# Optimization experiments

Hardware: AMD Instinct MI355X
Metric: run time of the kernel (lower is better)

The kernel has to match this reference:

```python
import jax, jax.numpy as jnp
import numpy as np

NOPE, ROPE, VDIM, QKD = 128, 64, 128, 192
H = 16
EPS = 1e-6
SCALING = QKD ** -0.5


def rms_norm(x, w):
    xf = x.astype(jnp.float32)
    var = jnp.mean(xf * xf, axis=-1, keepdims=True)
    return (w * (xf * jax.lax.rsqrt(var + EPS))).astype(x.dtype)


def rotate_half(x):
    d = x.shape[-1] // 2
    return jnp.concatenate((-x[..., d:], x[..., :d]), axis=-1)


def apply_rope(q, k, cos, sin):
    # cos/sin: [B,S,D] -> unsqueeze head dim
    cos = cos[:, None, :, :]
    sin = sin[:, None, :, :]
    return q * cos + rotate_half(q) * sin, k * cos + rotate_half(k) * sin


def setup_inputs() -> dict:
    key = jax.random.key(0)
    ks = jax.random.split(key, 8)
    B, S, D = 2, 2048, 2048
    pos = jnp.arange(S, dtype=jnp.float32)
    inv_freq = 1.0 / (10000.0 ** (jnp.arange(0, ROPE, 2, dtype=jnp.float32) / ROPE))
    ang = pos[:, None] * inv_freq[None, :]            # [S, ROPE/2]
    emb = jnp.concatenate([ang, ang], axis=-1)        # [S, ROPE]
    cos = jnp.broadcast_to(jnp.cos(emb)[None], (B, S, ROPE))
    sin = jnp.broadcast_to(jnp.sin(emb)[None], (B, S, ROPE))
    s = lambda k, shp, fan: jax.random.normal(k, shp, jnp.float32) * (fan ** -0.5)
    return {
        "hidden_states": jax.random.normal(ks[0], (B, S, D), jnp.float32),
        "cos": cos,
        "sin": sin,
        "q_a_W": s(ks[1], (1536, D), D),
        "q_a_norm_w": jnp.ones((1536,), jnp.float32),
        "q_b_W": s(ks[2], (H * QKD, 1536), 1536),
        "kv_a_W": s(ks[3], (512 + ROPE, D), D),
        "kv_a_norm_w": jnp.ones((512,), jnp.float32),
        "kv_b_W": s(ks[4], (H * (NOPE + VDIM), 512), 512),
        "o_W": s(ks[5], (D, H * VDIM), H * VDIM),
    }


def reference(hidden_states, cos, sin, q_a_W, q_a_norm_w, q_b_W, kv_a_W,
              kv_a_norm_w, kv_b_W, o_W):
    B, S, D = hidden_states.shape
    # low-rank Q path
    q = rms_norm(hidden_states @ q_a_W.T, q_a_norm_w) @ q_b_W.T   # [B,S,H*QKD]
    q = q.reshape(B, S, H, QKD).transpose(0, 2, 1, 3)             # [B,H,S,QKD]
    q_pass, q_rot = q[..., :NOPE], q[..., NOPE:]
    # compressed KV path
    ckv = hidden_states @ kv_a_W.T                                # [B,S,512+ROPE]
    k_lat, k_rot = ckv[..., :512], ckv[..., 512:]
    kv = rms_norm(k_lat, kv_a_norm_w) @ kv_b_W.T                  # [B,S,H*(NOPE+VDIM)]
    kv = kv.reshape(B, S, H, NOPE + VDIM).transpose(0, 2, 1, 3)   # [B,H,S,*]
    k_pass, v = kv[..., :NOPE], kv[..., NOPE:]
    k_rot = k_rot.reshape(B, 1, S, ROPE)
    q_rot, k_rot = apply_rope(q_rot, k_rot, cos, sin)
    k_rot = jnp.broadcast_to(k_rot, (B, H, S, ROPE))
    query = jnp.concatenate((q_pass, q_rot), axis=-1)             # [B,H,S,QKD]
    key = jnp.concatenate((k_pass, k_rot), axis=-1)
    # eager causal attention
    scores = jnp.einsum('bhsd,bhtd->bhst', query, key) * SCALING
    causal = jnp.tril(jnp.ones((S, S), bool))
    scores = jnp.where(causal, scores, jnp.finfo(scores.dtype).min)
    attn = jax.nn.softmax(scores.astype(jnp.float32), axis=-1).astype(query.dtype)
    out = jnp.einsum('bhst,bhtd->bhsd', attn, v)                  # [B,H,S,VDIM]
    out = out.transpose(0, 2, 1, 3).reshape(B, S, H * VDIM)
    return out @ o_W.T
```

## Files before the change

### kernel.cpp

```cpp
#include <hip/hip_runtime.h>
#include <hip/hip_bf16.h>


typedef __bf16 bf16x8 __attribute__((ext_vector_type(8)));
typedef float floatx4 __attribute__((ext_vector_type(4)));
#define BF16 __hip_bfloat16

static __device__ __forceinline__ BF16 f2b(float x) { return __float2bfloat16(x); }
static __device__ __forceinline__ unsigned short b2u(BF16 x) { return *(unsigned short*)&x; }
static __device__ __forceinline__ float fast_exp2(float x) { return __builtin_amdgcn_exp2f(x); }

template<int CTRL>
static __device__ __forceinline__ float dpp_mov(float x) {
  int xi = __builtin_bit_cast(int, x);
  int yi = __builtin_amdgcn_update_dpp(xi, xi, CTRL, 0xF, 0xF, false);
  return __builtin_bit_cast(float, yi);
}
static __device__ __forceinline__ float row_allmax(float x) {
  x = fmaxf(x, dpp_mov<0xB1>(x));
  x = fmaxf(x, dpp_mov<0x4E>(x));
  x = fmaxf(x, dpp_mov<0x141>(x));
  x = fmaxf(x, dpp_mov<0x140>(x));
  return x;
}
static __device__ __forceinline__ float row_allsum(float x) {
  x += dpp_mov<0xB1>(x);
  x += dpp_mov<0x4E>(x);
  x += dpp_mov<0x141>(x);
  x += dpp_mov<0x140>(x);
  return x;
}

static __device__ __forceinline__ void load_lds16(const BF16* g, BF16* l) {
  __builtin_amdgcn_global_load_lds((__attribute__((address_space(1))) void*)(void*)g,
                                   (__attribute__((address_space(3))) void*)(void*)l,
                                   16, 0, 0);
}

struct CastArgs {
  const float* src[6];
  BF16* dst[6];
  long n[6];
};
__global__ void cast_multi_k(CastArgs a) {
  int r = blockIdx.y;
  long n = a.n[r];
  const float* __restrict__ x = a.src[r];
  BF16* __restrict__ y = a.dst[r];
  for (long i = ((long)blockIdx.x * 256 + threadIdx.x) * 4; i + 3 < n;
       i += (long)gridDim.x * 1024) {
    float4 v = *(const float4*)(x + i);
    y[i+0] = f2b(v.x); y[i+1] = f2b(v.y); y[i+2] = f2b(v.z); y[i+3] = f2b(v.w);
  }
}

template<int OUT_MODE>
static __device__ __forceinline__ void gemm_body(
    const BF16* __restrict__ A, const BF16* __restrict__ B, void* __restrict__ C,
    int M, int N, int K, const float* __restrict__ cosb, const float* __restrict__ sinb,
    BF16* __restrict__ P1, BF16* __restrict__ P2, int bx, int by, BF16* As, BF16* Bs) {
  int tid = threadIdx.x, wave = tid >> 6, lane = tid & 63;
  int wr = wave >> 1, wc = wave & 1, lr = lane & 15, quad = lane >> 4;
  long m0 = (long)by * 128, n0 = (long)bx * 128;

  int c0 = wave*64 + lane, c1 = c0 + 256;
  const BF16* ga0 = A + (m0 + (c0>>2))*(long)K + (c0&3)*8;
  const BF16* ga1 = A + (m0 + (c1>>2))*(long)K + (c1&3)*8;
  long bn0 = n0 + (c0>>2); if (bn0 >= N) bn0 = N-1;
  long bn1 = n0 + (c1>>2); if (bn1 >= N) bn1 = N-1;
  const BF16* gb0 = B + bn0*(long)K + (c0&3)*8;
  const BF16* gb1 = B + bn1*(long)K + (c1&3)*8;
  BF16* la0 = As + wave*512;
  BF16* la1 = As + wave*512 + 2048;
  BF16* lb0 = Bs + wave*512;
  BF16* lb1 = Bs + wave*512 + 2048;

  floatx4 acc[4][4] = {};
  for (int k0 = 0; k0 < K; k0 += 32) {
    __syncthreads();
    load_lds16(ga0 + k0, la0);
    load_lds16(ga1 + k0, la1);
    load_lds16(gb0 + k0, lb0);
    load_lds16(gb1 + k0, lb1);
    __syncthreads();
    bf16x8 a[4], b[4];
#pragma unroll
    for (int i = 0; i < 4; i++) a[i] = *(const bf16x8*)(As + (wr*64 + i*16 + lr)*32 + quad*8);
#pragma unroll
    for (int j = 0; j < 4; j++) b[j] = *(const bf16x8*)(Bs + (wc*64 + j*16 + lr)*32 + quad*8);
#pragma unroll
    for (int i = 0; i < 4; i++)
#pragma unroll
      for (int j = 0; j < 4; j++)
        acc[i][j] = __builtin_amdgcn_mfma_f32_16x16x32_bf16(a[i], b[j], acc[i][j], 0, 0, 0);
  }

  long n0w = n0 + wc*64;
  const float SCALE_L2E = 0.104117546f;
#pragma unroll
  for (int i = 0; i < 4; i++) {
    long tok = m0 + wr*64 + i*16 + quad*4;
    long bb = tok >> 11, s = tok & 2047;
    if (OUT_MODE == 0) {
#pragma unroll
      for (int r = 0; r < 4; r++) {
        long row = tok + r;
#pragma unroll
        for (int j = 0; j < 4; j++) {
          long col = n0w + j*16 + lr;
          if (col < N) ((float*)C)[row*(long)N + col] = acc[i][j][r];
        }
      }
    } else if (OUT_MODE == 2) {
#pragma unroll
      for (int j = 0; j < 4; j++) {
        long col = n0w + j*16 + lr;
        long h = col >> 8, d = col & 255;
        if (d < 128) {
#pragma unroll
          for (int r = 0; r < 4; r++)
            P1[((bb*16 + h)*2048 + s + r)*192 + d] = f2b(acc[i][j][r]);
        } else {
          ushort4 pk;
          pk.x = b2u(f2b(acc[i][j][0])); pk.y = b2u(f2b(acc[i][j][1]));
          pk.z = b2u(f2b(acc[i][j][2])); pk.w = b2u(f2b(acc[i][j][3]));
          *(ushort4*)(P2 + ((bb*16 + h)*128 + d - 128)*2048 + s) = pk;
        }
      }
    } else {
      bool rope = ((n0w % 192) == 128);
#pragma unroll
      for (int r = 0; r < 4; r++) {
        long row = tok + r;
#pragma unroll
        for (int j = 0; j < 4; j++) {
          long col = n0w + j*16 + lr;
          float x = acc[i][j][r], val;
          if (rope) {
            int id = j*16 + lr;
            float partner = acc[i][j^2][r];
            float rot = (j < 2) ? -partner : partner;
            val = x*cosb[row*64 + id] + rot*sinb[row*64 + id];
          } else {
            val = x;
          }
          long h = col / 192, d = col % 192;
          P1[((bb*16 + h)*2048 + s + r)*192 + d] = f2b(val * SCALE_L2E);
        }
      }
    }
  }
}

__global__ __launch_bounds__(256) void gemm0_k(const BF16* __restrict__ A, const BF16* __restrict__ B,
                                               float* __restrict__ C, int M, int N, int K) {
  __shared__ __align__(16) BF16 As[128*32];
  __shared__ __align__(16) BF16 Bs[128*32];
  gemm_body<0>(A, B, C, M, N, K, nullptr, nullptr, nullptr, nullptr,
               blockIdx.x, blockIdx.y, As, Bs);
}

__global__ __launch_bounds__(256) void gemm_qkv_k(const BF16* __restrict__ qan, const BF16* __restrict__ Wqb,
                                                  const BF16* __restrict__ kvn, const BF16* __restrict__ Wkvb,
                                                  const float* __restrict__ cosb, const float* __restrict__ sinb,
                                                  BF16* __restrict__ Qt, BF16* __restrict__ Kt,
                                                  BF16* __restrict__ Vt) {
  __shared__ __align__(16) BF16 As[128*32];
  __shared__ __align__(16) BF16 Bs[128*32];
  int bid = blockIdx.x;
  if (bid < 768) {
    gemm_body<3>(qan, Wqb, nullptr, 4096, 3072, 1536, cosb, sinb, Qt, nullptr,
                 bid % 24, bid / 24, As, Bs);
  } else {
    bid -= 768;
    gemm_body<2>(kvn, Wkvb, nullptr, 4096, 4096, 512, nullptr, nullptr, Kt, Vt,
                 bid % 32, bid / 32, As, Bs);
  }
}

__global__ __launch_bounds__(256) void norms_k(const float* __restrict__ qakv,
                                               const float* __restrict__ qw, const float* __restrict__ kw,
                                               const float* __restrict__ cosb, const float* __restrict__ sinb,
                                               BF16* __restrict__ qan, BF16* __restrict__ kvn,
                                               BF16* __restrict__ Kt) {
  long row = blockIdx.x;
  const float* xr = qakv + row * 2112;
  int tid = threadIdx.x;
  __shared__ float red[4];
  {
    float ss = 0.f;
    for (int i = tid*4; i < 1536; i += 1024) {
      float4 v = *(const float4*)(xr + i);
      ss += v.x*v.x + v.y*v.y + v.z*v.z + v.w*v.w;
    }
#pragma unroll
    for (int off = 32; off > 0; off >>= 1) ss += __shfl_down(ss, off);
    if ((tid & 63) == 0) red[tid >> 6] = ss;
    __syncthreads();
    float rs = rsqrtf((red[0]+red[1]+red[2]+red[3]) / 1536.f + 1e-6f);
    BF16* yr = qan + row * 1536;
    for (int i = tid*4; i < 1536; i += 1024) {
      float4 v = *(const float4*)(xr + i);
      yr[i+0] = f2b(v.x * qw[i+0] * rs);
      yr[i+1] = f2b(v.y * qw[i+1] * rs);
      yr[i+2] = f2b(v.z * qw[i+2] * rs);
      yr[i+3] = f2b(v.w * qw[i+3] * rs);
    }
  }
  __syncthreads();
  {
    float ss = 0.f;
    for (int i = tid*4; i < 512; i += 1024) {
      float4 v = *(const float4*)(xr + 1536 + i);
      ss += v.x*v.x + v.y*v.y + v.z*v.z + v.w*v.w;
    }
#pragma unroll
    for (int off = 32; off > 0; off >>= 1) ss += __shfl_down(ss, off);
    if ((tid & 63) == 0) red[tid >> 6] = ss;
    __syncthreads();
    float rs = rsqrtf((red[0]+red[1]+red[2]+red[3]) / 512.f + 1e-6f);
    BF16* yr = kvn + row * 512;
    for (int i = tid*4; i < 512; i += 1024) {
      float4 v = *(const float4*)(xr + 1536 + i);
      yr[i+0] = f2b(v.x * kw[i+0] * rs);
      yr[i+1] = f2b(v.y * kw[i+1] * rs);
      yr[i+2] = f2b(v.z * kw[i+2] * rs);
      yr[i+3] = f2b(v.w * kw[i+3] * rs);
    }
  }
  if (tid < 64) {
    int i = tid;
    const float* kr = xr + 2048;
    float x = kr[i];
    float rot = (i < 32) ? -kr[i + 32] : kr[i - 32];
    BF16 v = f2b(x * cosb[row*64 + i] + rot * sinb[row*64 + i]);
    long b = row >> 11, s = row & 2047;
    long base = ((b*16)*2048 + s)*192 + 128 + i;
#pragma unroll
    for (int h = 0; h < 16; h++) Kt[base + (long)h*2048*192] = v;
  }
}

#define LK 200
#define LV 72
#define LP 72
__global__ __launch_bounds__(512) void flash_k(const BF16* __restrict__ Qt, const BF16* __restrict__ Kt,
                                               const BF16* __restrict__ Vt, BF16* __restrict__ O) {
  __shared__ __align__(16) BF16 Ks[64*LK];
  __shared__ __align__(16) BF16 Vs[128*LV];
  __shared__ __align__(16) BF16 Ps[8][16*LP];
  int tid = threadIdx.x, wave = tid >> 6, lane = tid & 63;
  int lr = lane & 15, quad = lane >> 4;
  int F = blockIdx.x;
  int g = F & 31, j = F >> 5;
  int h = g & 15, b = g >> 4;
  const BF16* Qb = Qt + ((long)(b*16 + h) * 2048) * 192;
  const BF16* Kb = Kt + ((long)(b*16 + h) * 2048) * 192;
  const BF16* Vb = Vt + ((long)(b*16 + h) * 128) * 2048;
  const float NEG_INF = -__builtin_inff();

  int krow[3], kcol[3];
#pragma unroll
  for (int i = 0; i < 3; i++) {
    int c = tid + 512*i;
    krow[i] = c / 24; kcol[i] = (c % 24) * 8;
  }
  int vrow[2], vcol[2];
#pragma unroll
  for (int i = 0; i < 2; i++) {
    int c = tid + 512*i;
    vrow[i] = c >> 3; vcol[i] = (c & 7) * 8;
  }

  bf16x8 kreg[3], vreg[2];
  auto stage_load = [&](int k0) {
#pragma unroll
    for (int i = 0; i < 3; i++)
      kreg[i] = *(const bf16x8*)(Kb + (long)(k0 + krow[i])*192 + kcol[i]);
#pragma unroll
    for (int i = 0; i < 2; i++)
      vreg[i] = *(const bf16x8*)(Vb + (long)vrow[i]*2048 + k0 + vcol[i]);
  };
  auto stage_store = [&]() {
#pragma unroll
    for (int i = 0; i < 3; i++)
      *(bf16x8*)(Ks + krow[i]*LK + kcol[i]) = kreg[i];
#pragma unroll
    for (int i = 0; i < 2; i++)
      *(bf16x8*)(Vs + vrow[i]*LV + vcol[i]) = vreg[i];
  };

  for (int half = 0; half < 2; half++) {
    int qt = (half == 0) ? j : 15 - j;
    int q0 = qt * 128;
    int wq0 = q0 + wave*16;
    bf16x8 qf[6];
    {
      const BF16* qp = Qb + (long)(wq0 + lr) * 192 + quad*8;
#pragma unroll
      for (int f = 0; f < 6; f++) qf[f] = *(const bf16x8*)(qp + f*32);
    }
    float m_i[4], l_i[4];
#pragma unroll
    for (int r = 0; r < 4; r++) { m_i[r] = NEG_INF; l_i[r] = 0.f; }
    floatx4 o_acc[8] = {};
    int nk = 2*qt + 2;
    stage_load(0);
    for (int kt = 0; kt < nk; kt++) {
      __syncthreads();
      stage_store();
      __syncthreads();
      if (kt + 1 < nk) stage_load((kt + 1) * 64);
      if (kt*64 > wq0 + 15) continue;
      floatx4 st[4];
#pragma unroll
      for (int t = 0; t < 4; t++) {
        floatx4 c = {};
#pragma unroll
        for (int f = 0; f < 6; f++) {
          bf16x8 kf = *(const bf16x8*)(Ks + (t*16+lr)*LK + f*32 + quad*8);
          c = __builtin_amdgcn_mfma_f32_16x16x32_bf16(qf[f], kf, c, 0, 0, 0);
        }
        st[t] = c;
      }
      float mt[4];
#pragma unroll
      for (int r = 0; r < 4; r++) mt[r] = NEG_INF;
      if (kt*64 + 63 > wq0) {
        int rbase = wq0 + quad*4 - kt*64;
#pragma unroll
        for (int t = 0; t < 4; t++) {
          int coff = t*16 + lr;
#pragma unroll
          for (int r = 0; r < 4; r++) {
            float sc = st[t][r];
            if (coff > rbase + r) sc = NEG_INF;
            st[t][r] = sc;
            mt[r] = fmaxf(mt[r], sc);
          }
        }
      } else {
#pragma unroll
        for (int t = 0; t < 4; t++)
#pragma unroll
          for (int r = 0; r < 4; r++) mt[r] = fmaxf(mt[r], st[t][r]);
      }
#pragma unroll
      for (int r = 0; r < 4; r++) mt[r] = row_allmax(mt[r]);
      float alpha[4], rsum[4];
#pragma unroll
      for (int r = 0; r < 4; r++) {
        float mn = fmaxf(m_i[r], mt[r]);
        alpha[r] = fast_exp2(m_i[r] - mn);
        m_i[r] = mn;
        rsum[r] = 0.f;
      }
#pragma unroll
      for (int t = 0; t < 4; t++)
#pragma unroll
        for (int r = 0; r < 4; r++) {
          float p = fast_exp2(st[t][r] - m_i[r]);
          st[t][r] = p;
          rsum[r] += p;
        }
#pragma unroll
      for (int r = 0; r < 4; r++) rsum[r] = row_allsum(rsum[r]);
#pragma unroll
      for (int r = 0; r < 4; r++) l_i[r] = l_i[r]*alpha[r] + rsum[r];
#pragma unroll
      for (int v = 0; v < 8; v++)
#pragma unroll
        for (int r = 0; r < 4; r++) o_acc[v][r] *= alpha[r];
#pragma unroll
      for (int t = 0; t < 4; t++)
#pragma unroll
        for (int r = 0; r < 4; r++)
          Ps[wave][(quad*4 + r)*LP + t*16 + lr] = f2b(st[t][r]);
#pragma unroll
      for (int kc = 0; kc < 2; kc++) {
        bf16x8 pa = *(const bf16x8*)(&Ps[wave][lr*LP + kc*32 + quad*8]);
#pragma unroll
        for (int v = 0; v < 8; v++) {
          bf16x8 vf = *(const bf16x8*)(&Vs[(v*16+lr)*LV + kc*32 + quad*8]);
          o_acc[v] = __builtin_amdgcn_mfma_f32_16x16x32_bf16(pa, vf, o_acc[v], 0, 0, 0);
        }
      }
    }
    long rowb = wq0 + quad*4;
#pragma unroll
    for (int v = 0; v < 8; v++)
#pragma unroll
      for (int r = 0; r < 4; r++) {
        long row = rowb + r;
        O[((long)b*2048 + row)*2048 + h*128 + v*16 + lr] = f2b(o_acc[v][r] / l_i[r]);
      }
  }
}

extern "C" void kernel_launch(void* const* d_in, const int* in_sizes, int n_in,
                              void* d_out, int out_size, void* d_ws, size_t ws_size,
                              hipStream_t stream) {
  const float* hidden      = (const float*)d_in[0];
  const float* cosb        = (const float*)d_in[1];
  const float* sinb        = (const float*)d_in[2];
  const float* q_a_W       = (const float*)d_in[3];
  const float* q_a_norm_w  = (const float*)d_in[4];
  const float* q_b_W       = (const float*)d_in[5];
  const float* kv_a_W      = (const float*)d_in[6];
  const float* kv_a_norm_w = (const float*)d_in[7];
  const float* kv_b_W      = (const float*)d_in[8];
  const float* o_W         = (const float*)d_in[9];
  float* out = (float*)d_out;

  const int Mrows = 4096;

  char* ws = (char*)d_ws; size_t off = 0;
  auto alloc = [&](size_t bytes) -> void* {
    void* p = ws + off; off = (off + bytes + 255) & ~(size_t)255; return p;
  };
  BF16* hb    = (BF16*)alloc((size_t)4096*2048*2);
  BF16* Wqakv = (BF16*)alloc((size_t)2112*2048*2);
  BF16* Wqb   = (BF16*)alloc((size_t)3072*1536*2);
  BF16* Wkvb  = (BF16*)alloc((size_t)4096*512*2);
  BF16* Wo    = (BF16*)alloc((size_t)2048*2048*2);
  float* qakv = (float*)alloc((size_t)4096*2112*4);
  BF16* qan   = (BF16*)alloc((size_t)4096*1536*2);
  BF16* kvn   = (BF16*)alloc((size_t)4096*512*2);
  BF16* Qt    = (BF16*)alloc((size_t)2*16*2048*192*2);
  BF16* Kt    = (BF16*)alloc((size_t)2*16*2048*192*2);
  BF16* Vt    = (BF16*)alloc((size_t)2*16*128*2048*2);
  BF16* attn  = (BF16*)alloc((size_t)4096*2048*2);

  CastArgs ca;
  ca.src[0] = hidden;  ca.dst[0] = hb;                 ca.n[0] = (long)4096*2048;
  ca.src[1] = q_a_W;   ca.dst[1] = Wqakv;              ca.n[1] = (long)1536*2048;
  ca.src[2] = kv_a_W;  ca.dst[2] = Wqakv + (long)1536*2048; ca.n[2] = (long)576*2048;
  ca.src[3] = q_b_W;   ca.dst[3] = Wqb;                ca.n[3] = (long)3072*1536;
  ca.src[4] = kv_b_W;  ca.dst[4] = Wkvb;               ca.n[4] = (long)4096*512;
  ca.src[5] = o_W;     ca.dst[5] = Wo;                 ca.n[5] = (long)2048*2048;
  cast_multi_k<<<dim3(1024, 6), dim3(256), 0, stream>>>(ca);

  gemm0_k<<<dim3(17, 32), dim3(256), 0, stream>>>(hb, Wqakv, qakv, Mrows, 2112, 2048);

  norms_k<<<dim3(4096), dim3(256), 0, stream>>>(qakv, q_a_norm_w, kv_a_norm_w,
                                                cosb, sinb, qan, kvn, Kt);

  gemm_qkv_k<<<dim3(1792), dim3(256), 0, stream>>>(qan, Wqb, kvn, Wkvb, cosb, sinb, Qt, Kt, Vt);

  flash_k<<<dim3(256), dim3(512), 0, stream>>>(Qt, Kt, Vt, attn);

  gemm0_k<<<dim3(16, 32), dim3(256), 0, stream>>>(attn, Wo, out, Mrows, 2048, 2048);
}
```

Before: 478.7 us.

## Double-buffer GEMM LDS tiles with XOR swizzle and 256x128 block tiles

Rewrites the shared GEMM body to use 512-thread blocks computing 256x128 tiles with a K-step of 64. Global-to-LDS loads for the next two K tiles are issued while the current tile is consumed, using vmcnt waits and raw barriers. An XOR swizzle is added to avoid LDS bank conflicts, and MFMA phases run at raised wave priority. The larger LDS footprint (96KB) and the higher register count can lower occupancy, and grid sizes shrink accordingly.

```diff
diff --git a/kernel.cpp b/kernel.cpp
--- a/kernel.cpp
+++ b/kernel.cpp
@@ -61,38 +61,87 @@
     BF16* __restrict__ P1, BF16* __restrict__ P2, int bx, int by, BF16* As, BF16* Bs) {
   int tid = threadIdx.x, wave = tid >> 6, lane = tid & 63;
   int wr = wave >> 1, wc = wave & 1, lr = lane & 15, quad = lane >> 4;
-  long m0 = (long)by * 128, n0 = (long)bx * 128;
-
-  int c0 = wave*64 + lane, c1 = c0 + 256;
-  const BF16* ga0 = A + (m0 + (c0>>2))*(long)K + (c0&3)*8;
-  const BF16* ga1 = A + (m0 + (c1>>2))*(long)K + (c1&3)*8;
-  long bn0 = n0 + (c0>>2); if (bn0 >= N) bn0 = N-1;
-  long bn1 = n0 + (c1>>2); if (bn1 >= N) bn1 = N-1;
-  const BF16* gb0 = B + bn0*(long)K + (c0&3)*8;
-  const BF16* gb1 = B + bn1*(long)K + (c1&3)*8;
-  BF16* la0 = As + wave*512;
-  BF16* la1 = As + wave*512 + 2048;
-  BF16* lb0 = Bs + wave*512;
-  BF16* lb1 = Bs + wave*512 + 2048;
+  long m0 = (long)by * 256, n0 = (long)bx * 128;
+
+  long asrc[4]; int adst[4];
+#pragma unroll
+  for (int i = 0; i < 4; i++) {
+    int c = wave*64 + lane + 512*i;
+    int r = c >> 3, k = c & 7;
+    asrc[i] = (m0 + r) * (long)K + ((k ^ (r & 7)) << 3);
+    adst[i] = wave*512 + i*4096;
+  }
+  long bsrc[2]; int bdst[2];
+#pragma unroll
+  for (int i = 0; i < 2; i++) {
+    int c = wave*64 + lane + 512*i;
+    int r = c >> 3, k = c & 7;
+    long bn = n0 + r; if (bn >= N) bn = N - 1;
+    bsrc[i] = bn * (long)K + ((k ^ (r & 7)) << 3);
+    bdst[i] = wave*512 + i*4096;
+  }
+
+  auto stage = [&](int bi, int kt) {
+    long k0 = (long)kt << 6;
+    BF16* Ad = As + bi*16384;
+    BF16* Bd = Bs + bi*8192;
+#pragma unroll
+    for (int i = 0; i < 4; i++) load_lds16(A + asrc[i] + k0, Ad + adst[i]);
+#pragma unroll
+    for (int i = 0; i < 2; i++) load_lds16(B + bsrc[i] + k0, Bd + bdst[i]);
+  };
+
+  int aoff[4], boff[4];
+#pragma unroll
+  for (int i = 0; i < 4; i++) aoff[i] = (wr*64 + i*16 + lr) * 64;
+#pragma unroll
+  for (int j = 0; j < 4; j++) boff[j] = (wc*64 + j*16 + lr) * 64;
+  int x0 = ((quad    ) ^ (lr & 7)) << 3;
+  int x1 = ((quad ^ 4) ^ (lr & 7)) << 3;
 
   floatx4 acc[4][4] = {};
-  for (int k0 = 0; k0 < K; k0 += 32) {
-    __syncthreads();
-    load_lds16(ga0 + k0, la0);
-    load_lds16(ga1 + k0, la1);
-    load_lds16(gb0 + k0, lb0);
-    load_lds16(gb1 + k0, lb1);
-    __syncthreads();
-    bf16x8 a[4], b[4];
-#pragma unroll
-    for (int i = 0; i < 4; i++) a[i] = *(const bf16x8*)(As + (wr*64 + i*16 + lr)*32 + quad*8);
-#pragma unroll
-    for (int j = 0; j < 4; j++) b[j] = *(const bf16x8*)(Bs + (wc*64 + j*16 + lr)*32 + quad*8);
+  int NT = K >> 6;
+
+  stage(0, 0);
+  stage(1, 1);
+  asm volatile("s_waitcnt vmcnt(6)" ::: "memory");
+  __builtin_amdgcn_s_barrier();
+
+  int cur = 0;
+  for (int t = 0; t < NT; t++) {
+    const BF16* Ab = As + cur*16384;
+    const BF16* Bb = Bs + cur*8192;
+    bf16x8 a0[4], a1[4], b0[4], b1[4];
+#pragma unroll
+    for (int i = 0; i < 4; i++) {
+      a0[i] = *(const bf16x8*)(Ab + aoff[i] + x0);
+      a1[i] = *(const bf16x8*)(Ab + aoff[i] + x1);
+    }
+#pragma unroll
+    for (int j = 0; j < 4; j++) {
+      b0[j] = *(const bf16x8*)(Bb + boff[j] + x0);
+      b1[j] = *(const bf16x8*)(Bb + boff[j] + x1);
+    }
+    asm volatile("s_waitcnt lgkmcnt(0)" ::: "memory");
+    __builtin_amdgcn_s_barrier();
+    if (t + 2 < NT) stage(cur, t + 2);
+    __builtin_amdgcn_s_setprio(1);
 #pragma unroll
     for (int i = 0; i < 4; i++)
 #pragma unroll
       for (int j = 0; j < 4; j++)
-        acc[i][j] = __builtin_amdgcn_mfma_f32_16x16x32_bf16(a[i], b[j], acc[i][j], 0, 0, 0);
+        acc[i][j] = __builtin_amdgcn_mfma_f32_16x16x32_bf16(a0[i], b0[j], acc[i][j], 0, 0, 0);
+#pragma unroll
+    for (int i = 0; i < 4; i++)
+#pragma unroll
+      for (int j = 0; j < 4; j++)
+        acc[i][j] = __builtin_amdgcn_mfma_f32_16x16x32_bf16(a1[i], b1[j], acc[i][j], 0, 0, 0);
+    __builtin_amdgcn_s_setprio(0);
+    if (t + 2 < NT)      { asm volatile("s_waitcnt vmcnt(6)" ::: "memory"); }
+    else if (t + 1 < NT) { asm volatile("s_waitcnt vmcnt(0)" ::: "memory"); }
+    __builtin_amdgcn_s_barrier();
+    __builtin_amdgcn_sched_barrier(0);
+    cur ^= 1;
   }
 
   long n0w = n0 + wc*64;
@@ -152,27 +201,27 @@
   }
 }
 
-__global__ __launch_bounds__(256) void gemm0_k(const BF16* __restrict__ A, const BF16* __restrict__ B,
+__global__ __launch_bounds__(512) void gemm0_k(const BF16* __restrict__ A, const BF16* __restrict__ B,
                                                float* __restrict__ C, int M, int N, int K) {
-  __shared__ __align__(16) BF16 As[128*32];
-  __shared__ __align__(16) BF16 Bs[128*32];
+  __shared__ __align__(16) BF16 As[2*256*64];
+  __shared__ __align__(16) BF16 Bs[2*128*64];
   gemm_body<0>(A, B, C, M, N, K, nullptr, nullptr, nullptr, nullptr,
                blockIdx.x, blockIdx.y, As, Bs);
 }
 
-__global__ __launch_bounds__(256) void gemm_qkv_k(const BF16* __restrict__ qan, const BF16* __restrict__ Wqb,
+__global__ __launch_bounds__(512) void gemm_qkv_k(const BF16* __restrict__ qan, const BF16* __restrict__ Wqb,
                                                   const BF16* __restrict__ kvn, const BF16* __restrict__ Wkvb,
                                                   const float* __restrict__ cosb, const float* __restrict__ sinb,
                                                   BF16* __restrict__ Qt, BF16* __restrict__ Kt,
                                                   BF16* __restrict__ Vt) {
-  __shared__ __align__(16) BF16 As[128*32];
-  __shared__ __align__(16) BF16 Bs[128*32];
+  __shared__ __align__(16) BF16 As[2*256*64];
+  __shared__ __align__(16) BF16 Bs[2*128*64];
   int bid = blockIdx.x;
-  if (bid < 768) {
+  if (bid < 384) {
     gemm_body<3>(qan, Wqb, nullptr, 4096, 3072, 1536, cosb, sinb, Qt, nullptr,
                  bid % 24, bid / 24, As, Bs);
   } else {
-    bid -= 768;
+    bid -= 384;
     gemm_body<2>(kvn, Wkvb, nullptr, 4096, 4096, 512, nullptr, nullptr, Kt, Vt,
                  bid % 32, bid / 32, As, Bs);
   }
@@ -440,14 +489,14 @@
   ca.src[5] = o_W;     ca.dst[5] = Wo;                 ca.n[5] = (long)2048*2048;
   cast_multi_k<<<dim3(1024, 6), dim3(256), 0, stream>>>(ca);
 
-  gemm0_k<<<dim3(17, 32), dim3(256), 0, stream>>>(hb, Wqakv, qakv, Mrows, 2112, 2048);
+  gemm0_k<<<dim3(17, 16), dim3(512), 0, stream>>>(hb, Wqakv, qakv, Mrows, 2112, 2048);
 
   norms_k<<<dim3(4096), dim3(256), 0, stream>>>(qakv, q_a_norm_w, kv_a_norm_w,
                                                 cosb, sinb, qan, kvn, Kt);
 
-  gemm_qkv_k<<<dim3(1792), dim3(256), 0, stream>>>(qan, Wqb, kvn, Wkvb, cosb, sinb, Qt, Kt, Vt);
+  gemm_qkv_k<<<dim3(896), dim3(512), 0, stream>>>(qan, Wqb, kvn, Wkvb, cosb, sinb, Qt, Kt, Vt);
 
   flash_k<<<dim3(256), dim3(512), 0, stream>>>(Qt, Kt, Vt, attn);
 
-  gemm0_k<<<dim3(16, 32), dim3(256), 0, stream>>>(attn, Wo, out, Mrows, 2048, 2048);
-}
+  gemm0_k<<<dim3(16, 16), dim3(512), 0, stream>>>(attn, Wo, out, Mrows, 2048, 2048);
+}
```

After: 450.9 us. -5.8%, faster.
